# Kernel optimization log

Hardware: AMD Instinct MI355X
Metric: run time of the kernel (lower is better)

## Reference

```python
import jax, jax.numpy as jnp
import numpy as np

EMBED = 256; G = 8; NC = 6; NL = 4; NP = 13
BS = 1; NA = 900
IMG_W, IMG_H = 704.0, 256.0
LEVEL_HW = [(64, 176), (32, 88), (16, 44), (8, 22)]


def setup_inputs() -> dict:
    key = jax.random.key(0)
    ks = jax.random.split(key, 12)
    inp = {}
    inp["instance_feature"] = jax.random.normal(ks[0], (BS, NA, EMBED), jnp.float32)
    inp["anchor_embed"] = jax.random.normal(ks[1], (BS, NA, EMBED), jnp.float32)
    # key points in normalized [0,1) cube; projection matrix maps them to pixel coords
    inp["key_points"] = jax.random.uniform(ks[2], (BS, NA, NP, 3), jnp.float32)
    for i, (h, w) in enumerate(LEVEL_HW):
        inp[f"fm{i}"] = jax.random.normal(ks[3 + i], (BS, NC, EMBED, h, w), jnp.float32)
    # intrinsics-like projection: x->x*W, y->y*H, depth ~ z+0.5, plus per-camera jitter
    base = jnp.array([[IMG_W, 0.0, 0.0, 0.0],
                      [0.0, IMG_H, 0.0, 0.0],
                      [0.0, 0.0, 1.0, 0.5],
                      [0.0, 0.0, 0.0, 1.0]], jnp.float32)
    inp["projection_mat"] = base[None, None] + 0.05 * jax.random.normal(ks[7], (BS, NC, 4, 4), jnp.float32)
    inp["image_wh"] = jnp.broadcast_to(jnp.array([IMG_W, IMG_H], jnp.float32), (BS, NC, 2))
    inp["w_weights"] = 0.02 * jax.random.normal(ks[8], (EMBED, G * NC * NL * NP), jnp.float32)
    inp["b_weights"] = jnp.zeros((G * NC * NL * NP,), jnp.float32)
    inp["w_out"] = 0.02 * jax.random.normal(ks[9], (EMBED, EMBED), jnp.float32)
    inp["b_out"] = jnp.zeros((EMBED,), jnp.float32)
    return inp


def _grid_sample(fm, grid):
    # fm: (B, C, H, W); grid: (B, A, P, 2) in [-1,1]. Bilinear, zero padding,
    # align_corners=False (torch F.grid_sample defaults). Returns (B, A, P, C).
    B, C, H, W = fm.shape
    A, P = grid.shape[1], grid.shape[2]
    gx = (grid[..., 0] + 1.0) * (W * 0.5) - 0.5
    gy = (grid[..., 1] + 1.0) * (H * 0.5) - 0.5
    x0 = jnp.floor(gx); y0 = jnp.floor(gy)
    fmf = jnp.transpose(fm.reshape(B, C, H * W), (0, 2, 1))  # (B, HW, C)

    def gather(xi, yi):
        valid = (xi >= 0) & (xi <= W - 1) & (yi >= 0) & (yi <= H - 1)
        xc = jnp.clip(xi, 0, W - 1).astype(jnp.int32)
        yc = jnp.clip(yi, 0, H - 1).astype(jnp.int32)
        idx = (yc * W + xc).reshape(B, A * P, 1)
        g = jnp.take_along_axis(fmf, idx, axis=1).reshape(B, A, P, C)
        return g * valid[..., None].astype(fm.dtype)

    wx1 = gx - x0; wx0 = 1.0 - wx1
    wy1 = gy - y0; wy0 = 1.0 - wy1
    return (gather(x0, y0) * (wx0 * wy0)[..., None]
            + gather(x0 + 1.0, y0) * (wx1 * wy0)[..., None]
            + gather(x0, y0 + 1.0) * (wx0 * wy1)[..., None]
            + gather(x0 + 1.0, y0 + 1.0) * (wx1 * wy1)[..., None])


def reference(instance_feature, anchor_embed, key_points, fm0, fm1, fm2, fm3,
              projection_mat, image_wh, w_weights, b_weights, w_out, b_out):
    bs, na = instance_feature.shape[:2]
    gd = EMBED // G
    # _get_weights: softmax over (cams*levels*pts) jointly, per group
    feat = instance_feature + anchor_embed
    w = (feat @ w_weights + b_weights).reshape(bs, na, NC * NL * NP, G)
    w = jax.nn.softmax(w, axis=2).reshape(bs, na, NC, NL, NP, G)
    # feature_sampling: project 3D key points to each camera's pixel plane
    kp_h = jnp.concatenate([key_points, jnp.ones_like(key_points[..., :1])], axis=-1)
    p2 = jnp.einsum('bcij,banj->bcani', projection_mat, kp_h)  # (bs,cams,na,pts,4)
    xy = p2[..., :2] / jnp.maximum(p2[..., 2:3], 1e-5)
    grid = (xy / image_wh[:, :, None, None]) * 2.0 - 1.0
    grid = grid.reshape(bs * NC, na, NP, 2)
    # bilinear sample every pyramid level for every camera
    feats = jnp.stack([
        _grid_sample(fm.reshape(bs * NC, EMBED, fm.shape[-2], fm.shape[-1]), grid)
        for fm in (fm0, fm1, fm2, fm3)
    ], axis=0)  # (L, bs*cams, na, pts, E)
    feats = feats.reshape(NL, bs, NC, na, NP, G, gd)
    # multi_view_level_fusion: weighted sum over cams and levels, per group
    fused = jnp.einsum('baclpg,lbcapgd->bapgd', w, feats).reshape(bs, na, NP, EMBED)
    out = fused.sum(axis=2)  # sum over key points
    return out @ w_out + b_out + instance_feature  # output_proj + residual 'add'
```

## Files before the change

kernel.cpp:

```cpp
#include <hip/hip_runtime.h>
#include <hip/hip_bf16.h>
#include <hip/hip_fp16.h>
#include <cstdint>

#define EMBED 256
#define GPS 8
#define NCAM 6
#define NLVL 4
#define NPT 13
#define NANC 900
#define NSAMP (NCAM*NLVL*NPT)
#define NWCOL (GPS*NSAMP)
#define MPAD 928
#define WSTRIDE 328
#define MAXENT 352

#define FMOFF0 0
#define FMOFF1 17301504
#define FMOFF2 21626880
#define FMOFF3 22708224
#define TALL_BYTES 22978560

typedef __attribute__((ext_vector_type(8))) short bf16x8;
typedef __attribute__((ext_vector_type(16))) float f32x16;
typedef __attribute__((ext_vector_type(2))) float v2f;

__device__ __forceinline__ ushort bf16bits(float x) {
    __hip_bfloat16 h = __float2bfloat16(x);
    return *reinterpret_cast<ushort*>(&h);
}

__global__ __launch_bounds__(256) void k_prep(
        const float* __restrict__ fm0, const float* __restrict__ fm1,
        const float* __restrict__ fm2, const float* __restrict__ fm3,
        unsigned char* __restrict__ t0, unsigned char* __restrict__ t1,
        unsigned char* __restrict__ t2, unsigned char* __restrict__ t3,
        const float* __restrict__ wlin, __hip_bfloat16* __restrict__ wt,
        const float* __restrict__ inst, const float* __restrict__ anch,
        __hip_bfloat16* __restrict__ featB,
        const float* __restrict__ kp, const float* __restrict__ proj,
        float* __restrict__ pxy) {
    __shared__ ushort lds2[128 * 64];
    int b = blockIdx.x;
    int t = threadIdx.x;
    if (b < 1404) {
        const float* in; unsigned char* outp; int HW, chunks, lb;
        if (b < 1056)      { in = fm0; outp = t0; HW = 11264; chunks = 176; lb = b; }
        else if (b < 1320) { in = fm1; outp = t1; HW = 2816;  chunks = 44;  lb = b - 1056; }
        else if (b < 1386) { in = fm2; outp = t2; HW = 704;   chunks = 11;  lb = b - 1320; }
        else               { in = fm3; outp = t3; HW = 176;   chunks = 3;   lb = b - 1386; }
        int c = lb / chunks;
        int hw0 = (lb - c * chunks) * 64;
        int q = t & 15, eg = t >> 4;
        bool vld = (hw0 + q * 4 + 3) < HW;
        const float* srcq = in + (size_t)c * EMBED * HW + hw0 + q * 4;
        float4 vals[16];
        #pragma unroll
        for (int r = 0; r < 16; r++) {
            int e = 2 * eg + (r & 1) + 32 * (r >> 1);
            vals[r] = vld ? *(const float4*)(srcq + (size_t)e * HW)
                          : make_float4(0.f, 0.f, 0.f, 0.f);
        }
        #pragma unroll
        for (int rp = 0; rp < 8; rp++) {
            int ep = eg + 16 * rp;
            int s2 = (ep >> 1) & 62;
            float4 va = vals[2 * rp], vb = vals[2 * rp + 1];
            uint p0 = (uint)__builtin_amdgcn_cvt_pk_fp8_f32(va.x, vb.x, 0, false) & 0xffff;
            uint p1 = (uint)__builtin_amdgcn_cvt_pk_fp8_f32(va.y, vb.y, 0, false) & 0xffff;
            uint p2 = (uint)__builtin_amdgcn_cvt_pk_fp8_f32(va.z, vb.z, 0, false) & 0xffff;
            uint p3 = (uint)__builtin_amdgcn_cvt_pk_fp8_f32(va.w, vb.w, 0, false) & 0xffff;
            int col01 = (q * 4) ^ s2;
            int col23 = (q * 4 + 2) ^ s2;
            *reinterpret_cast<uint*>(&lds2[ep * 64 + col01]) = p0 | (p1 << 16);
            *reinterpret_cast<uint*>(&lds2[ep * 64 + col23]) = p2 | (p3 << 16);
        }
        __syncthreads();
        ushort* outb = reinterpret_cast<ushort*>(outp) + ((size_t)c * HW + hw0) * 128;
        #pragma unroll
        for (int r = 0; r < 8; r++) {
            int flat = r * 2048 + t * 8;
            int hw = flat >> 8;
            int ep0 = (flat & 255) >> 1;
            if (hw0 + hw < HW) {
                ushort4 u;
                #pragma unroll
                for (int j = 0; j < 4; j++) {
                    int ep = ep0 + j;
                    int s2 = (ep >> 1) & 62;
                    u[j] = lds2[ep * 64 + (hw ^ s2)];
                }
                *reinterpret_cast<ushort4*>(outb + flat / 2) = u;
            }
        }
    } else if (b < 1560) {
        int b1 = b - 1404;
        int kt = b1 / 39, nt = b1 - kt * 39;
        int k0 = kt * 64, n0 = nt * 64;
        int grp = t >> 6, nn = t & 63;
        #pragma unroll
        for (int r = 0; r < 16; r++) {
            int kk = grp * 16 + r;
            lds2[kk * 65 + nn] = bf16bits(wlin[(size_t)(k0 + kk) * NWCOL + n0 + nn]);
        }
        __syncthreads();
        ushort* wtb = reinterpret_cast<ushort*>(wt);
        int kk2 = t & 63;
        #pragma unroll
        for (int r = 0; r < 16; r++) {
            int nn2 = grp * 16 + r;
            wtb[(size_t)(n0 + nn2) * EMBED + k0 + kk2] = lds2[kk2 * 65 + nn2];
        }
    } else if (b < 1785) {
        int base = (b - 1560) * 1024 + t * 4;
        float4 a = *(const float4*)&inst[base];
        float4 c = *(const float4*)&anch[base];
        ushort4 r;
        r.x = bf16bits(a.x + c.x); r.y = bf16bits(a.y + c.y);
        r.z = bf16bits(a.z + c.z); r.w = bf16bits(a.w + c.w);
        *reinterpret_cast<ushort4*>(reinterpret_cast<ushort*>(featB) + base) = r;
    } else if (b < 1792) {
        int base = 900 * EMBED + (b - 1785) * 1024 + t * 4;
        ushort4 z; z.x = z.y = z.z = z.w = 0;
        *reinterpret_cast<ushort4*>(reinterpret_cast<ushort*>(featB) + base) = z;
    } else {
        int i = (b - 1792) * 256 + t;
        if (i < NANC * NCAM * NPT) {
            int a = i / (NCAM * NPT);
            int r = i - a * (NCAM * NPT);
            int c = r / NPT;
            int p = r - c * NPT;
            const float* M = proj + c * 16;
            const float* k3 = kp + ((size_t)a * NPT + p) * 3;
            float kx = k3[0], ky = k3[1], kz = k3[2];
            float X = M[0] * kx + M[1] * ky + M[2] * kz + M[3];
            float Y = M[4] * kx + M[5] * ky + M[6] * kz + M[7];
            float Z = M[8] * kx + M[9] * ky + M[10] * kz + M[11];
            float invz = 1.f / fmaxf(Z, 1e-5f);
            pxy[(size_t)i * 2 + 0] = X * invz;
            pxy[(size_t)i * 2 + 1] = Y * invz;
        }
    }
}

#define MT 29
#define NT 78
__global__ __launch_bounds__(256) void k_gemm(const __hip_bfloat16* __restrict__ featB,
                                              const __hip_bfloat16* __restrict__ wt,
                                              const float* __restrict__ blin,
                                              float* __restrict__ logits) {
    int wv = threadIdx.x >> 6, lane = threadIdx.x & 63;
    int idx = blockIdx.x * 4 + wv;
    if (idx >= MT * NT) return;
    int mt = idx % MT, nt = idx / MT;
    int m0 = mt * 32, n0 = nt * 32;
    int l31 = lane & 31;
    int khalf = (lane >> 5) * 8;
    const short* ap = reinterpret_cast<const short*>(featB) + (size_t)(m0 + l31) * EMBED + khalf;
    const short* bp = reinterpret_cast<const short*>(wt)    + (size_t)(n0 + l31) * EMBED + khalf;
    f32x16 acc = {};
    #pragma unroll 8
    for (int ki = 0; ki < 16; ki++) {
        bf16x8 a = *reinterpret_cast<const bf16x8*>(ap + ki * 16);
        bf16x8 bb = *reinterpret_cast<const bf16x8*>(bp + ki * 16);
        acc = __builtin_amdgcn_mfma_f32_32x32x16_bf16(a, bb, acc, 0, 0, 0);
    }
    float bias = blin[n0 + l31];
    int colg = n0 + l31;
    #pragma unroll
    for (int r = 0; r < 16; r++) {
        int row = (r & 3) + 8 * (r >> 2) + 4 * (lane >> 5);
        int grow = m0 + row;
        if (grow < NANC)
            logits[(size_t)grow * NWCOL + colg] = acc[r] + bias;
    }
}

__global__ __launch_bounds__(512) void k_aggregate(const unsigned char* __restrict__ tAll,
                                                   const float* __restrict__ logits,
                                                   const float* __restrict__ pxy,
                                                   const float* __restrict__ wout,
                                                   const float* __restrict__ bout,
                                                   const float* __restrict__ inst,
                                                   float* __restrict__ out) {
    __shared__ float wT[GPS * WSTRIDE];
    __shared__ float xyS[NCAM * NPT * 2];
    __shared__ float redS[8][EMBED];
    __shared__ float pS[EMBED];
    __shared__ float rsS[GPS];
    __shared__ int4  eOff[MAXENT];
    __shared__ float4 eW[MAXENT];
    __shared__ int   eS[MAXENT];
    __shared__ int   cntS;
    int a = blockIdx.x;
    int tid = threadIdx.x;
    int wave = tid >> 6;
    int lane = tid & 63;
    if (tid == 0) cntS = 0;
    for (int j = tid; j < NWCOL; j += 512)
        wT[(j & 7) * WSTRIDE + (j >> 3)] = logits[(size_t)a * NWCOL + j];
    for (int j = tid; j < NCAM * NPT * 2; j += 512)
        xyS[j] = pxy[(size_t)a * NCAM * NPT * 2 + j];
    __syncthreads();
    {
        int g = wave;
        float m = -1e30f;
        for (int s = lane; s < NSAMP; s += 64) m = fmaxf(m, wT[g * WSTRIDE + s]);
        #pragma unroll
        for (int off = 32; off; off >>= 1) m = fmaxf(m, __shfl_xor(m, off));
        float ssum = 0.f;
        for (int s = lane; s < NSAMP; s += 64) {
            float e = __expf(wT[g * WSTRIDE + s] - m);
            wT[g * WSTRIDE + s] = e;
            ssum += e;
        }
        #pragma unroll
        for (int off = 32; off; off >>= 1) ssum += __shfl_xor(ssum, off);
        if (lane == 0) rsS[g] = 1.f / ssum;
    }
    {
        bool valid = false; int4 o4; float4 w4;
        if (tid < NSAMP) {
            int c = tid / 52, rem = tid - c * 52;
            int l = rem / 13, p = rem - l * 13;
            float X = xyS[(c * NPT + p) * 2], Y = xyS[(c * NPT + p) * 2 + 1];
            int Wl = 176 >> l, Hl = 64 >> l;
            float scale = 0.25f / (float)(1 << l);
            float gx = fmaf(X, scale, -0.5f);
            float gy = fmaf(Y, scale, -0.5f);
            float x0f = floorf(gx), y0f = floorf(gy);
            float fx = gx - x0f, fy = gy - y0f;
            int x0 = (int)x0f, y0 = (int)y0f;
            int x1 = x0 + 1, y1 = y0 + 1;
            bool vx0 = (x0 >= 0) && (x0 < Wl);
            bool vx1 = (x1 >= 0) && (x1 < Wl);
            bool vy0 = (y0 >= 0) && (y0 < Hl);
            bool vy1 = (y1 >= 0) && (y1 < Hl);
            w4.x = (vx0 && vy0) ? (1.f - fx) * (1.f - fy) : 0.f;
            w4.y = (vx1 && vy0) ? fx * (1.f - fy) : 0.f;
            w4.z = (vx0 && vy1) ? (1.f - fx) * fy : 0.f;
            w4.w = (vx1 && vy1) ? fx * fy : 0.f;
            if (w4.x + w4.y + w4.z + w4.w > 0.f) {
                valid = true;
                int xc0 = min(max(x0, 0), Wl - 1), xc1 = min(max(x1, 0), Wl - 1);
                int yc0 = min(max(y0, 0), Hl - 1), yc1 = min(max(y1, 0), Hl - 1);
                const int lvlBase[4] = { FMOFF0, FMOFF1, FMOFF2, FMOFF3 };
                int cb = lvlBase[l] + c * (Wl * Hl) * EMBED;
                o4.x = cb + (yc0 * Wl + xc0) * EMBED;
                o4.y = cb + (yc0 * Wl + xc1) * EMBED;
                o4.z = cb + (yc1 * Wl + xc0) * EMBED;
                o4.w = cb + (yc1 * Wl + xc1) * EMBED;
            }
        }
        unsigned long long mask = __ballot(valid);
        int prefix = __popcll(mask & ((1ull << lane) - 1ull));
        int wcount = __popcll(mask);
        int basev = 0;
        if (lane == 0 && wcount) basev = atomicAdd(&cntS, wcount);
        basev = __shfl(basev, 0);
        if (valid) {
            int pos = basev + prefix;
            eOff[pos] = o4; eW[pos] = w4; eS[pos] = tid;
        }
    }
    __syncthreads();
    int cnt = cntS;
    int cnt_pad = (cnt + 31) & ~31;
    for (int j = cnt + tid; j < cnt_pad; j += 512) {
        eOff[j] = make_int4(0, 0, 0, 0);
        eW[j] = make_float4(0.f, 0.f, 0.f, 0.f);
        eS[j] = 0;
    }
    __syncthreads();
    int half = lane >> 5;
    int hl = lane & 31;
    int ch0 = hl * 8;
    int g = hl >> 2;
    float acc0 = 0.f, acc1 = 0.f, acc2 = 0.f, acc3 = 0.f;
    float acc4 = 0.f, acc5 = 0.f, acc6 = 0.f, acc7 = 0.f;
    auto consume = [&](const float4& w, int sIdx,
                       uint2 c0, uint2 c1, uint2 c2, uint2 c3) {
        float wg = wT[g * WSTRIDE + sIdx];
        float w0 = wg * w.x, w1 = wg * w.y, w2 = wg * w.z, w3 = wg * w.w;
        v2f p;
        p = __builtin_amdgcn_cvt_pk_f32_fp8(c0.x, false); acc0 = fmaf(w0, p.x, acc0); acc1 = fmaf(w0, p.y, acc1);
        p = __builtin_amdgcn_cvt_pk_f32_fp8(c0.x, true);  acc2 = fmaf(w0, p.x, acc2); acc3 = fmaf(w0, p.y, acc3);
        p = __builtin_amdgcn_cvt_pk_f32_fp8(c0.y, false); acc4 = fmaf(w0, p.x, acc4); acc5 = fmaf(w0, p.y, acc5);
        p = __builtin_amdgcn_cvt_pk_f32_fp8(c0.y, true);  acc6 = fmaf(w0, p.x, acc6); acc7 = fmaf(w0, p.y, acc7);
        p = __builtin_amdgcn_cvt_pk_f32_fp8(c1.x, false); acc0 = fmaf(w1, p.x, acc0); acc1 = fmaf(w1, p.y, acc1);
        p = __builtin_amdgcn_cvt_pk_f32_fp8(c1.x, true);  acc2 = fmaf(w1, p.x, acc2); acc3 = fmaf(w1, p.y, acc3);
        p = __builtin_amdgcn_cvt_pk_f32_fp8(c1.y, false); acc4 = fmaf(w1, p.x, acc4); acc5 = fmaf(w1, p.y, acc5);
        p = __builtin_amdgcn_cvt_pk_f32_fp8(c1.y, true);  acc6 = fmaf(w1, p.x, acc6); acc7 = fmaf(w1, p.y, acc7);
        p = __builtin_amdgcn_cvt_pk_f32_fp8(c2.x, false); acc0 = fmaf(w2, p.x, acc0); acc1 = fmaf(w2, p.y, acc1);
        p = __builtin_amdgcn_cvt_pk_f32_fp8(c2.x, true);  acc2 = fmaf(w2, p.x, acc2); acc3 = fmaf(w2, p.y, acc3);
        p = __builtin_amdgcn_cvt_pk_f32_fp8(c2.y, false); acc4 = fmaf(w2, p.x, acc4); acc5 = fmaf(w2, p.y, acc5);
        p = __builtin_amdgcn_cvt_pk_f32_fp8(c2.y, true);  acc6 = fmaf(w2, p.x, acc6); acc7 = fmaf(w2, p.y, acc7);
        p = __builtin_amdgcn_cvt_pk_f32_fp8(c3.x, false); acc0 = fmaf(w3, p.x, acc0); acc1 = fmaf(w3, p.y, acc1);
        p = __builtin_amdgcn_cvt_pk_f32_fp8(c3.x, true);  acc2 = fmaf(w3, p.x, acc2); acc3 = fmaf(w3, p.y, acc3);
        p = __builtin_amdgcn_cvt_pk_f32_fp8(c3.y, false); acc4 = fmaf(w3, p.x, acc4); acc5 = fmaf(w3, p.y, acc5);
        p = __builtin_amdgcn_cvt_pk_f32_fp8(c3.y, true);  acc6 = fmaf(w3, p.x, acc6); acc7 = fmaf(w3, p.y, acc7);
    };
    int steps = cnt_pad >> 4;
    if (steps > 0) {
        int ei = wave * 2 + half;
        int4 oA = eOff[ei]; float4 wA = eW[ei]; int sA = eS[ei];
        uint2 vA0 = *(const uint2*)(tAll + oA.x + ch0);
        uint2 vA1 = *(const uint2*)(tAll + oA.y + ch0);
        uint2 vA2 = *(const uint2*)(tAll + oA.z + ch0);
        uint2 vA3 = *(const uint2*)(tAll + oA.w + ch0);
        for (int it = 0; it < steps; it += 2) {
            int ej = ei + 16;
            int4 oB = eOff[ej]; float4 wB = eW[ej]; int sB = eS[ej];
            uint2 vB0 = *(const uint2*)(tAll + oB.x + ch0);
            uint2 vB1 = *(const uint2*)(tAll + oB.y + ch0);
            uint2 vB2 = *(const uint2*)(tAll + oB.z + ch0);
            uint2 vB3 = *(const uint2*)(tAll + oB.w + ch0);
            consume(wA, sA, vA0, vA1, vA2, vA3);
            ei = ej + 16;
            if (it + 2 < steps) {
                oA = eOff[ei]; wA = eW[ei]; sA = eS[ei];
                vA0 = *(const uint2*)(tAll + oA.x + ch0);
                vA1 = *(const uint2*)(tAll + oA.y + ch0);
                vA2 = *(const uint2*)(tAll + oA.z + ch0);
                vA3 = *(const uint2*)(tAll + oA.w + ch0);
            }
            consume(wB, sB, vB0, vB1, vB2, vB3);
        }
    }
    acc0 += __shfl_xor(acc0, 32); acc1 += __shfl_xor(acc1, 32);
    acc2 += __shfl_xor(acc2, 32); acc3 += __shfl_xor(acc3, 32);
    acc4 += __shfl_xor(acc4, 32); acc5 += __shfl_xor(acc5, 32);
    acc6 += __shfl_xor(acc6, 32); acc7 += __shfl_xor(acc7, 32);
    if (half == 0) {
        redS[wave][ch0 + 0] = acc0; redS[wave][ch0 + 1] = acc1;
        redS[wave][ch0 + 2] = acc2; redS[wave][ch0 + 3] = acc3;
        redS[wave][ch0 + 4] = acc4; redS[wave][ch0 + 5] = acc5;
        redS[wave][ch0 + 6] = acc6; redS[wave][ch0 + 7] = acc7;
    }
    __syncthreads();
    int col = tid & 255;
    int kh = tid >> 8;
    if (kh == 0) {
        float s = redS[0][col] + redS[1][col] + redS[2][col] + redS[3][col]
                + redS[4][col] + redS[5][col] + redS[6][col] + redS[7][col];
        redS[0][col] = s * rsS[col >> 5];
    }
    __syncthreads();
    float acc = 0.f;
    int kbase = kh * 128;
    #pragma unroll 8
    for (int k = 0; k < 128; k++)
        acc = fmaf(redS[0][kbase + k], wout[(size_t)(kbase + k) * EMBED + col], acc);
    if (kh == 1) pS[col] = acc;
    __syncthreads();
    if (kh == 0)
        out[(size_t)a * EMBED + col] = acc + pS[col] + bout[col] + inst[(size_t)a * EMBED + col];
}

extern "C" void kernel_launch(void* const* d_in, const int* in_sizes, int n_in,
                              void* d_out, int out_size, void* d_ws, size_t ws_size,
                              hipStream_t stream) {
    const float* inst = (const float*)d_in[0];
    const float* anch = (const float*)d_in[1];
    const float* kp   = (const float*)d_in[2];
    const float* fm0  = (const float*)d_in[3];
    const float* fm1  = (const float*)d_in[4];
    const float* fm2  = (const float*)d_in[5];
    const float* fm3  = (const float*)d_in[6];
    const float* proj = (const float*)d_in[7];
    const float* wlin = (const float*)d_in[9];
    const float* blin = (const float*)d_in[10];
    const float* wout = (const float*)d_in[11];
    const float* bout = (const float*)d_in[12];
    float* out = (float*)d_out;

    char* ws = (char*)d_ws;
    size_t off = 0;
    auto alloc = [&](size_t bytes) -> void* {
        void* p = ws + off;
        off = (off + bytes + 255) & ~(size_t)255;
        return p;
    };
    unsigned char* tAll = (unsigned char*)alloc((size_t)TALL_BYTES);
    unsigned char* t0 = tAll + FMOFF0;
    unsigned char* t1 = tAll + FMOFF1;
    unsigned char* t2 = tAll + FMOFF2;
    unsigned char* t3 = tAll + FMOFF3;
    __hip_bfloat16* wt    = (__hip_bfloat16*)alloc((size_t)NWCOL * EMBED * 2);
    __hip_bfloat16* featB = (__hip_bfloat16*)alloc((size_t)MPAD * EMBED * 2);
    float* logits = (float*)alloc((size_t)NANC * NWCOL * 4);
    float* pxy    = (float*)alloc((size_t)NANC * NCAM * NPT * 2 * 4);

    k_prep<<<dim3(2067), 256, 0, stream>>>(fm0, fm1, fm2, fm3, t0, t1, t2, t3,
                                           wlin, wt, inst, anch, featB, kp, proj, pxy);
    k_gemm<<<dim3((MT * NT + 3) / 4), 256, 0, stream>>>(featB, wt, blin, logits);
    k_aggregate<<<dim3(NANC), 512, 0, stream>>>(tAll, logits, pxy,
                                                wout, bout, inst, out);
}
```

Baseline: 198.6 us.

## Split output projection into separate fp16 MFMA GEMM kernel and store logits as fp16

The per-anchor scalar output projection (256x256 FMA loop reading w_out in fp32 inside k_aggregate) is removed. The aggregate kernel now writes fp16 fused features, and a new k_out kernel runs the projection as a batched fp16 MFMA GEMM with bias and residual added. w_out is transposed and converted to fp16 in extra k_prep blocks. Logits are also stored as fp16, halving their write/read traffic, at the cost of an extra launch and some precision loss in the softmax inputs and the projection.

New measurement: 197.6 us. No clear change (-0.5%).

```diff
diff --git a/kernel.cpp b/kernel.cpp
--- a/kernel.cpp
+++ b/kernel.cpp
@@ -22,11 +22,16 @@
 #define TALL_BYTES 22978560
 
 typedef __attribute__((ext_vector_type(8))) short bf16x8;
+typedef __attribute__((ext_vector_type(8))) _Float16 f16x8;
 typedef __attribute__((ext_vector_type(16))) float f32x16;
 typedef __attribute__((ext_vector_type(2))) float v2f;
 
 __device__ __forceinline__ ushort bf16bits(float x) {
     __hip_bfloat16 h = __float2bfloat16(x);
+    return *reinterpret_cast<ushort*>(&h);
+}
+__device__ __forceinline__ ushort f16bits(float x) {
+    _Float16 h = (_Float16)x;
     return *reinterpret_cast<ushort*>(&h);
 }
 
@@ -39,7 +44,8 @@
         const float* __restrict__ inst, const float* __restrict__ anch,
         __hip_bfloat16* __restrict__ featB,
         const float* __restrict__ kp, const float* __restrict__ proj,
-        float* __restrict__ pxy) {
+        float* __restrict__ pxy,
+        const float* __restrict__ wout, ushort* __restrict__ woutT) {
     __shared__ ushort lds2[128 * 64];
     int b = blockIdx.x;
     int t = threadIdx.x;
@@ -123,7 +129,7 @@
         int base = 900 * EMBED + (b - 1785) * 1024 + t * 4;
         ushort4 z; z.x = z.y = z.z = z.w = 0;
         *reinterpret_cast<ushort4*>(reinterpret_cast<ushort*>(featB) + base) = z;
-    } else {
+    } else if (b < 2067) {
         int i = (b - 1792) * 256 + t;
         if (i < NANC * NCAM * NPT) {
             int a = i / (NCAM * NPT);
@@ -140,6 +146,23 @@
             pxy[(size_t)i * 2 + 0] = X * invz;
             pxy[(size_t)i * 2 + 1] = Y * invz;
         }
+    } else {
+        int b1 = b - 2067;
+        int kt = b1 >> 2, nt = b1 & 3;
+        int k0 = kt * 64, n0 = nt * 64;
+        int grp = t >> 6, nn = t & 63;
+        #pragma unroll
+        for (int r = 0; r < 16; r++) {
+            int kk = grp * 16 + r;
+            lds2[kk * 65 + nn] = f16bits(wout[(size_t)(k0 + kk) * EMBED + n0 + nn]);
+        }
+        __syncthreads();
+        int kk2 = t & 63;
+        #pragma unroll
+        for (int r = 0; r < 16; r++) {
+            int nn2 = grp * 16 + r;
+            woutT[(size_t)(n0 + nn2) * EMBED + k0 + kk2] = lds2[kk2 * 65 + nn2];
+        }
     }
 }
 
@@ -148,7 +171,7 @@
 __global__ __launch_bounds__(256) void k_gemm(const __hip_bfloat16* __restrict__ featB,
                                               const __hip_bfloat16* __restrict__ wt,
                                               const float* __restrict__ blin,
-                                              float* __restrict__ logits) {
+                                              _Float16* __restrict__ logits) {
     int wv = threadIdx.x >> 6, lane = threadIdx.x & 63;
     int idx = blockIdx.x * 4 + wv;
     if (idx >= MT * NT) return;
@@ -172,21 +195,17 @@
         int row = (r & 3) + 8 * (r >> 2) + 4 * (lane >> 5);
         int grow = m0 + row;
         if (grow < NANC)
-            logits[(size_t)grow * NWCOL + colg] = acc[r] + bias;
+            logits[(size_t)grow * NWCOL + colg] = (_Float16)(acc[r] + bias);
     }
 }
 
 __global__ __launch_bounds__(512) void k_aggregate(const unsigned char* __restrict__ tAll,
-                                                   const float* __restrict__ logits,
+                                                   const _Float16* __restrict__ logits,
                                                    const float* __restrict__ pxy,
-                                                   const float* __restrict__ wout,
-                                                   const float* __restrict__ bout,
-                                                   const float* __restrict__ inst,
-                                                   float* __restrict__ out) {
+                                                   _Float16* __restrict__ fusedH) {
     __shared__ float wT[GPS * WSTRIDE];
     __shared__ float xyS[NCAM * NPT * 2];
     __shared__ float redS[8][EMBED];
-    __shared__ float pS[EMBED];
     __shared__ float rsS[GPS];
     __shared__ int4  eOff[MAXENT];
     __shared__ float4 eW[MAXENT];
@@ -198,7 +217,7 @@
     int lane = tid & 63;
     if (tid == 0) cntS = 0;
     for (int j = tid; j < NWCOL; j += 512)
-        wT[(j & 7) * WSTRIDE + (j >> 3)] = logits[(size_t)a * NWCOL + j];
+        wT[(j & 7) * WSTRIDE + (j >> 3)] = (float)logits[(size_t)a * NWCOL + j];
     for (int j = tid; j < NCAM * NPT * 2; j += 512)
         xyS[j] = pxy[(size_t)a * NCAM * NPT * 2 + j];
     __syncthreads();
@@ -338,23 +357,46 @@
         redS[wave][ch0 + 6] = acc6; redS[wave][ch0 + 7] = acc7;
     }
     __syncthreads();
-    int col = tid & 255;
-    int kh = tid >> 8;
-    if (kh == 0) {
+    if (tid < EMBED) {
+        int col = tid;
         float s = redS[0][col] + redS[1][col] + redS[2][col] + redS[3][col]
                 + redS[4][col] + redS[5][col] + redS[6][col] + redS[7][col];
-        redS[0][col] = s * rsS[col >> 5];
-    }
-    __syncthreads();
-    float acc = 0.f;
-    int kbase = kh * 128;
+        fusedH[(size_t)a * EMBED + col] = (_Float16)(s * rsS[col >> 5]);
+    }
+}
+
+#define MT2 29
+#define NT2 8
+__global__ __launch_bounds__(256) void k_out(const _Float16* __restrict__ fusedH,
+                                             const _Float16* __restrict__ woutT,
+                                             const float* __restrict__ bout,
+                                             const float* __restrict__ inst,
+                                             float* __restrict__ out) {
+    int wv = threadIdx.x >> 6, lane = threadIdx.x & 63;
+    int idx = blockIdx.x * 4 + wv;
+    if (idx >= MT2 * NT2) return;
+    int mt = idx % MT2, nt = idx / MT2;
+    int m0 = mt * 32, n0 = nt * 32;
+    int l31 = lane & 31;
+    int khalf = (lane >> 5) * 8;
+    const _Float16* ap = fusedH + (size_t)(m0 + l31) * EMBED + khalf;
+    const _Float16* bp = woutT  + (size_t)(n0 + l31) * EMBED + khalf;
+    f32x16 acc = {};
     #pragma unroll 8
-    for (int k = 0; k < 128; k++)
-        acc = fmaf(redS[0][kbase + k], wout[(size_t)(kbase + k) * EMBED + col], acc);
-    if (kh == 1) pS[col] = acc;
-    __syncthreads();
-    if (kh == 0)
-        out[(size_t)a * EMBED + col] = acc + pS[col] + bout[col] + inst[(size_t)a * EMBED + col];
+    for (int ki = 0; ki < 16; ki++) {
+        f16x8 a  = *reinterpret_cast<const f16x8*>(ap + ki * 16);
+        f16x8 bb = *reinterpret_cast<const f16x8*>(bp + ki * 16);
+        acc = __builtin_amdgcn_mfma_f32_32x32x16_f16(a, bb, acc, 0, 0, 0);
+    }
+    int colg = n0 + l31;
+    float bias = bout[colg];
+    #pragma unroll
+    for (int r = 0; r < 16; r++) {
+        int row = (r & 3) + 8 * (r >> 2) + 4 * (lane >> 5);
+        int grow = m0 + row;
+        if (grow < NANC)
+            out[(size_t)grow * EMBED + colg] = acc[r] + bias + inst[(size_t)grow * EMBED + colg];
+    }
 }
 
 extern "C" void kernel_launch(void* const* d_in, const int* in_sizes, int n_in,
@@ -388,12 +430,16 @@
     unsigned char* t3 = tAll + FMOFF3;
     __hip_bfloat16* wt    = (__hip_bfloat16*)alloc((size_t)NWCOL * EMBED * 2);
     __hip_bfloat16* featB = (__hip_bfloat16*)alloc((size_t)MPAD * EMBED * 2);
-    float* logits = (float*)alloc((size_t)NANC * NWCOL * 4);
-    float* pxy    = (float*)alloc((size_t)NANC * NCAM * NPT * 2 * 4);
-
-    k_prep<<<dim3(2067), 256, 0, stream>>>(fm0, fm1, fm2, fm3, t0, t1, t2, t3,
-                                           wlin, wt, inst, anch, featB, kp, proj, pxy);
+    _Float16* logits = (_Float16*)alloc((size_t)NANC * NWCOL * 2);
+    float* pxy       = (float*)alloc((size_t)NANC * NCAM * NPT * 2 * 4);
+    _Float16* fusedH = (_Float16*)alloc((size_t)MPAD * EMBED * 2);
+    ushort* woutT    = (ushort*)alloc((size_t)EMBED * EMBED * 2);
+
+    k_prep<<<dim3(2083), 256, 0, stream>>>(fm0, fm1, fm2, fm3, t0, t1, t2, t3,
+                                           wlin, wt, inst, anch, featB, kp, proj, pxy,
+                                           wout, woutT);
     k_gemm<<<dim3((MT * NT + 3) / 4), 256, 0, stream>>>(featB, wt, blin, logits);
-    k_aggregate<<<dim3(NANC), 512, 0, stream>>>(tAll, logits, pxy,
-                                                wout, bout, inst, out);
-}
+    k_aggregate<<<dim3(NANC), 512, 0, stream>>>(tAll, logits, pxy, fusedH);
+    k_out<<<dim3((MT2 * NT2 + 3) / 4), 256, 0, stream>>>(fusedH, (const _Float16*)woutT,
+                                                         bout, inst, out);
+}
```
